# Kernel optimization log

Measured on AMD Instinct MI355X. Metric: run time of the kernel, lower is better.

Reference implementation:

```python
import jax, jax.numpy as jnp
import numpy as np
from jax import lax

EPS = 1e-10
DELU_P = 10.0

def delu(x):
    # delu_feature_map: param*relu(x) + (exp(param*min(x,0)) - 1) + 1
    x1 = jax.nn.relu(x)
    x2 = jnp.exp(DELU_P * (x - x1)) - 1.0
    return DELU_P * x1 + x2 + 1.0

def conv1x1(x, w, b):
    # x: (B,C,H,W), w: (O,C), b: (O,)
    return jnp.einsum('bchw,oc->bohw', x, w) + b[None, :, None, None]

def conv3x3(x, w, b):
    # w: (O,I,3,3), SAME padding, stride 1
    y = lax.conv_general_dilated(x, w, window_strides=(1, 1), padding='SAME',
                                 dimension_numbers=('NCHW', 'OIHW', 'NCHW'))
    return y + b[None, :, None, None]

def setup_inputs() -> dict:
    key = jax.random.key(0)
    ks = jax.random.split(key, 12)
    B, C, H, W = 4, 256, 128, 128
    s = 0.02
    return {
        'x':   jax.random.normal(ks[0], (B, C, H, W), dtype=jnp.float32),
        'wq':  jax.random.normal(ks[1], (C, C), dtype=jnp.float32) * s,
        'bq':  jax.random.normal(ks[2], (C,), dtype=jnp.float32) * s,
        'wk':  jax.random.normal(ks[3], (C, C), dtype=jnp.float32) * s,
        'bk':  jax.random.normal(ks[4], (C,), dtype=jnp.float32) * s,
        'wv':  jax.random.normal(ks[5], (C, C), dtype=jnp.float32) * s,
        'bv':  jax.random.normal(ks[6], (C,), dtype=jnp.float32) * s,
        'wd1': jax.random.normal(ks[7], (C, C), dtype=jnp.float32) * s,
        'bd1': jax.random.normal(ks[8], (C,), dtype=jnp.float32) * s,
        'wd3': jax.random.normal(ks[9], (C, C, 3, 3), dtype=jnp.float32) * s,
        'bd3': jax.random.normal(ks[10], (C,), dtype=jnp.float32) * s,
        'gamma': jax.random.normal(ks[11], (1,), dtype=jnp.float32) * 0.1,
    }

def reference(x, wq, bq, wk, bk, wv, bv, wd1, bd1, wd3, bd3, gamma):
    B, C, H, W = x.shape
    N = H * W
    # q/k/v projections flattened to (B, C, N)
    q = conv1x1(x, wq, bq).reshape(B, C, N)
    k = conv1x1(x, wk, bk).reshape(B, C, N)
    v = conv1x1(x, wv, bv).reshape(B, C, N)
    # feature maps (torch permutes q to (B,N,C), applies map, permutes back -> elementwise, no-op layout)
    q = delu(q)
    k = delu(k)
    # energy: (B, C, C), contracting over spatial N (q indexed 'bmn')
    energy = jnp.einsum('bmn,bcn->bmc', q, k)
    KV = k * v  # (B, C, N) elementwise
    norm = 1.0 / (jnp.einsum('bmc,bcn->bn', energy, k) + EPS)  # (B, N)
    # attention: sum over m of energy, times KV, times norm -> (B, C, N)
    attention = jnp.einsum('bmc,bcn,bn->bcn', energy, KV, norm)
    out = attention.reshape(B, C, H, W)
    out = out + conv1x1(x, wd1, bd1) + conv3x3(x, wd3, bd3)
    return x + gamma[0] * out
```

## Files before the change

### kernel.cpp

```cpp
#include <hip/hip_runtime.h>

#define BB 4
#define CC 256
#define HH 128
#define WW 128
#define NN (HH*WW)
#define EPSF 1e-10f

#define XR 130
#define XPB ((size_t)XR*XR*CC)

typedef __bf16 bf16x8 __attribute__((ext_vector_type(8)));
typedef float  f32x4  __attribute__((ext_vector_type(4)));
typedef float  f32x16 __attribute__((ext_vector_type(16)));

__device__ __forceinline__ float delu_f(float v) {
    return v > 0.0f ? fmaf(10.0f, v, 1.0f) : __expf(10.0f * v);
}

__device__ __forceinline__ void gl_lds16(const __bf16* g, __bf16* l) {
    __builtin_amdgcn_global_load_lds(
        (const __attribute__((address_space(1))) void*)g,
        (__attribute__((address_space(3))) void*)l, 16, 0, 0);
}

__global__ __launch_bounds__(256) void k_prep(const float* __restrict__ wq,
    const float* __restrict__ wk, const float* __restrict__ wv,
    const float* __restrict__ wd1, const float* __restrict__ wd3,
    __bf16* __restrict__ wqb, __bf16* __restrict__ wkb, __bf16* __restrict__ wvb,
    __bf16* __restrict__ wcv32)
{
    int idx = blockIdx.x * 256 + threadIdx.x;
    if (idx >= CC*CC) return;
    const int oc = idx >> 8, ic = idx & 255;
    const int ocf32 = oc >> 5;
    const int gks = ic >> 4, khi = (ic >> 3) & 1;
    const int lane32 = khi*32 + (oc & 31);
    const int e = ic & 7;
    const size_t off32 = ((size_t)(gks*8 + ocf32)*64 + lane32)*8 + e;
    wqb[off32] = (__bf16)wq[idx];
    wkb[off32] = (__bf16)wk[idx];
    wvb[off32] = (__bf16)wv[idx];
    float w9[9];
    #pragma unroll
    for (int k=0;k<9;k++) w9[k] = wd3[(size_t)idx*9 + k];
    w9[4] += wd1[idx];
    #pragma unroll
    for (int t=0;t<9;t++) wcv32[(size_t)t*CC*CC + off32] = (__bf16)w9[t];
}

__global__ __launch_bounds__(256) void k_xpad(const float* __restrict__ x,
                                              __bf16* __restrict__ xpad)
{
    const int xrow = blockIdx.x;
    const int b    = blockIdx.y;
    const int tid  = threadIdx.x;
    const int hr   = xrow - 1;
    const float* xb = x + (size_t)b*CC*NN;
    __bf16* xpb = xpad + (size_t)b*XPB + (size_t)xrow*XR*CC;
    const bool rowok = (hr >= 0 && hr < HH);
    for (int t = tid; t < XR*32; t += 256) {
        int xcol = t % XR, icg = t / XR;
        int wc = xcol - 1;
        bf16x8 v8 = {};
        if (rowok && wc >= 0 && wc < WW) {
            const float* p = xb + (size_t)(icg*8)*NN + hr*WW + wc;
            #pragma unroll
            for (int j=0;j<8;j++) v8[j] = (__bf16)p[(size_t)j*NN];
        }
        *(bf16x8*)&xpb[(size_t)xcol*CC + icg*8] = v8;
    }
}

__device__ __forceinline__ void stage_row128(const __bf16* __restrict__ xrb,
                                             __bf16* __restrict__ xs,
                                             int wid, int lane)
{
    #pragma unroll
    for (int j = 0; j < 16; ++j) {
        const int it = wid + 4*j;
        const int kq = it >> 1, ch = it & 1;
        gl_lds16(xrb + (size_t)(ch*64 + lane)*CC + kq*8, &xs[(size_t)(kq*132 + ch*64)*8]);
    }
}

__device__ __forceinline__ void mfma_gemm32(const __bf16* __restrict__ wb,
                                            const __bf16* __restrict__ xs,
                                            int wid, int lane, int l31, int lhi,
                                            f32x16 acc[2][4])
{
    #pragma unroll
    for (int kb=0; kb<8; kb++) {
        bf16x8 af[4];
        #pragma unroll
        for (int f=0; f<2; f++)
            #pragma unroll
            for (int kk=0; kk<2; kk++)
                af[f*2+kk] = *(const bf16x8*)&wb[((size_t)((kb*2+kk)*8 + wid*2 + f)*64 + lane)*8];
        #pragma unroll
        for (int kk=0; kk<2; kk++)
            #pragma unroll
            for (int nf=0; nf<4; nf++) {
                bf16x8 br = *(const bf16x8*)&xs[(size_t)((kb*4 + kk*2 + lhi)*132 + nf*32 + l31)*8];
                #pragma unroll
                for (int f=0; f<2; f++)
                    acc[f][nf] = __builtin_amdgcn_mfma_f32_32x32x16_bf16(af[f*2+kk], br, acc[f][nf], 0, 0, 0);
            }
    }
}

__global__ __launch_bounds__(256) void k_qk_mfma(const __bf16* __restrict__ xpad,
    const __bf16* __restrict__ wqb, const float* __restrict__ bq,
    const __bf16* __restrict__ wkb, const float* __restrict__ bk,
    __bf16* __restrict__ kp, float* __restrict__ Qs)
{
    __shared__ __bf16 xs[32*132*8];
    __shared__ float Qpart[4][128];
    const int h  = blockIdx.x;
    const int n0 = h * 128;
    const int b  = blockIdx.y;
    const int tid = threadIdx.x;
    const int wid = tid >> 6, lane = tid & 63;
    const int l31 = lane & 31, lhi = lane >> 5;
    const int oc_base = wid*64;
    const __bf16* xrb = xpad + (size_t)b*XPB + ((size_t)(h+1)*XR + 1)*CC;

    stage_row128(xrb, xs, wid, lane);
    __syncthreads();

    f32x16 acc[2][4] = {};
    mfma_gemm32(wqb, xs, wid, lane, l31, lhi, acc);
    #pragma unroll
    for (int nf=0; nf<4; nf++) {
        float s = 0.0f;
        #pragma unroll
        for (int f=0; f<2; f++)
            #pragma unroll
            for (int reg=0; reg<16; reg++) {
                const int oc = oc_base + f*32 + (reg&3) + 8*(reg>>2) + 4*lhi;
                s += delu_f(acc[f][nf][reg] + bq[oc]);
            }
        s += __shfl_xor(s, 32);
        if (lhi == 0) Qpart[wid][nf*32 + l31] = s;
    }
    __syncthreads();
    if (tid < 128)
        Qs[(size_t)b*NN + n0 + tid] = Qpart[0][tid] + Qpart[1][tid] + Qpart[2][tid] + Qpart[3][tid];

    #pragma unroll
    for (int f=0; f<2; f++)
        #pragma unroll
        for (int nf=0; nf<4; nf++)
            acc[f][nf] = (f32x16){};
    mfma_gemm32(wkb, xs, wid, lane, l31, lhi, acc);
    #pragma unroll
    for (int f=0; f<2; f++) {
        #pragma unroll
        for (int reg=0; reg<16; reg++) {
            const int oc = oc_base + f*32 + (reg&3) + 8*(reg>>2) + 4*lhi;
            const float bias = bk[oc];
            __bf16* kr = kp + ((size_t)b*CC + oc)*NN + n0;
            #pragma unroll
            for (int nf=0; nf<4; nf++)
                kr[nf*32 + l31] = (__bf16)delu_f(acc[f][nf][reg] + bias);
        }
    }
}

__global__ __launch_bounds__(256) void k_esum(const __bf16* __restrict__ kp,
    const float* __restrict__ Qs, float* __restrict__ Es)
{
    const int c = blockIdx.x & (CC-1), b = blockIdx.x >> 8;
    const int tid = threadIdx.x;
    const bf16x8* kr = (const bf16x8*)(kp + ((size_t)b*CC + c)*NN);
    const float4* qr = (const float4*)(Qs + (size_t)b*NN);
    float s = 0.0f;
    for (int i = tid; i < NN/8; i += 256) {
        bf16x8 kk = kr[i];
        float4 q0 = qr[2*i], q1 = qr[2*i+1];
        s += (float)kk[0]*q0.x + (float)kk[1]*q0.y + (float)kk[2]*q0.z + (float)kk[3]*q0.w
           + (float)kk[4]*q1.x + (float)kk[5]*q1.y + (float)kk[6]*q1.z + (float)kk[7]*q1.w;
    }
    #pragma unroll
    for (int m=1; m<64; m<<=1) s += __shfl_xor(s, m, 64);
    __shared__ float red[4];
    if ((tid & 63) == 0) red[tid >> 6] = s;
    __syncthreads();
    if (tid == 0) Es[b*CC + c] = red[0] + red[1] + red[2] + red[3];
}

__global__ __launch_bounds__(256,2) void k_conv_mfma(const __bf16* __restrict__ xpad,
    const __bf16* __restrict__ wcv32, const float* __restrict__ bd1,
    const float* __restrict__ bd3, __bf16* __restrict__ convout)
{
    __shared__ __bf16 xs[2][12*132*8];
    const int orig = blockIdx.x;
    const int wg   = (orig & 7)*64 + (orig >> 3);
    const int b    = wg >> 7;
    const int h    = wg & 127;
    const int tid = threadIdx.x;
    const int wid = tid >> 6, lane = tid & 63;
    const int l31 = lane & 31, lhi = lane >> 5;
    const int oc_base = wid*64;
    const __bf16* xpb = xpad + (size_t)b*XPB;

    f32x16 acc[2][4] = {};

    #define STAGE_CV(bufsel, icb) do {                                          \
        const int ic0_ = (icb)*32;                                              \
        _Pragma("unroll")                                                       \
        for (int j = 0; j < 9; ++j) {                                           \
            const int w_ = wid + 4*j;                                           \
            const int pair_ = w_ / 3, chunk_ = w_ % 3;                          \
            const int r_ = pair_ >> 2, icq_ = pair_ & 3;                        \
            const int col0_ = chunk_ * 64;                                      \
            if (col0_ + lane < XR)                                              \
                gl_lds16(xpb + ((size_t)(h + r_)*XR + col0_ + lane)*CC + ic0_ + icq_*8, \
                         &xs[bufsel][(size_t)(pair_*132 + col0_)*8]);           \
        }                                                                       \
    } while (0)

    #define AF_LOAD(dst, t, icb)                                                \
        _Pragma("unroll")                                                       \
        for (int f=0; f<2; f++)                                                 \
            _Pragma("unroll")                                                   \
            for (int kk=0; kk<2; kk++)                                          \
                dst[f*2+kk] = *(const bf16x8*)&wcv32[((size_t)(t)*CC*CC) +      \
                    ((size_t)((((icb)*2 + kk)*8 + wid*2 + f))*64 + lane)*8];

    STAGE_CV(0, 0);
    __syncthreads();

    #pragma unroll 1
    for (int icb = 0; icb < 8; ++icb) {
        bf16x8 af2[2][4];
        AF_LOAD(af2[0], 0, icb);
        if (icb < 7) STAGE_CV((icb+1)&1, icb+1);
        #pragma unroll
        for (int t=0; t<9; ++t) {
            const int cur = t & 1, nxt = cur ^ 1;
            const int ky = t/3, kx = t%3;
            if (t < 8) { AF_LOAD(af2[nxt], t+1, icb); }
            __builtin_amdgcn_s_setprio(1);
            #pragma unroll
            for (int kk=0; kk<2; kk++) {
                #pragma unroll
                for (int nf=0; nf<4; nf++) {
                    bf16x8 br = *(const bf16x8*)&xs[icb & 1][
                        (size_t)((ky*4 + kk*2 + lhi)*132 + nf*32 + l31 + kx)*8];
                    #pragma unroll
                    for (int f=0; f<2; f++)
                        acc[f][nf] = __builtin_amdgcn_mfma_f32_32x32x16_bf16(
                            af2[cur][f*2+kk], br, acc[f][nf], 0, 0, 0);
                }
            }
            __builtin_amdgcn_s_setprio(0);
        }
        __syncthreads();
    }
    #undef STAGE_CV
    #undef AF_LOAD

    #pragma unroll
    for (int f=0; f<2; f++) {
        #pragma unroll
        for (int reg=0; reg<16; reg++) {
            const int row = (reg & 3) + 8*(reg >> 2) + 4*lhi;
            const int oc = oc_base + f*32 + row;
            const float bias = bd1[oc] + bd3[oc];
            __bf16* orow = convout + ((size_t)b*CC + oc)*NN + (size_t)h*WW;
            #pragma unroll
            for (int nf=0; nf<4; nf++) {
                const int w = nf*32 + l31;
                orow[w] = (__bf16)(acc[f][nf][reg] + bias);
            }
        }
    }
}

__global__ __launch_bounds__(256) void k_vattn_mfma(
    const __bf16* __restrict__ xpad,
    const __bf16* __restrict__ wvb, const float* __restrict__ bv,
    const __bf16* __restrict__ kp, const float* __restrict__ Es,
    const __bf16* __restrict__ convout,
    const float* __restrict__ gamma, float* __restrict__ out)
{
    __shared__ __bf16 xs[32*132*8];
    __shared__ float Dpart[4][128];
    __shared__ float rn_sh[128];
    const int h  = blockIdx.x;
    const int n0 = h * 128;
    const int b  = blockIdx.y;
    const int tid = threadIdx.x;
    const int wid = tid >> 6, lane = tid & 63;
    const int l31 = lane & 31, lhi = lane >> 5;
    const int oc_base = wid*64;
    const __bf16* xrb = xpad + (size_t)b*XPB + ((size_t)(h+1)*XR + 1)*CC;

    stage_row128(xrb, xs, wid, lane);
    __syncthreads();

    f32x16 acc[2][4] = {};
    mfma_gemm32(wvb, xs, wid, lane, l31, lhi, acc);

    float dpart[4] = {0.f,0.f,0.f,0.f};
    #pragma unroll
    for (int f=0; f<2; f++) {
        #pragma unroll
        for (int reg=0; reg<16; reg++) {
            const int oc = oc_base + f*32 + (reg&3) + 8*(reg>>2) + 4*lhi;
            const float e = Es[b*CC + oc];
            const __bf16* kr = kp + ((size_t)b*CC + oc)*NN + n0;
            #pragma unroll
            for (int nf=0; nf<4; nf++)
                dpart[nf] = fmaf(e, (float)kr[nf*32 + l31], dpart[nf]);
        }
    }
    #pragma unroll
    for (int nf=0; nf<4; nf++) {
        dpart[nf] += __shfl_xor(dpart[nf], 32);
        if (lhi == 0) Dpart[wid][nf*32 + l31] = dpart[nf];
    }
    __syncthreads();
    if (tid < 128)
        rn_sh[tid] = 1.0f / (Dpart[0][tid] + Dpart[1][tid] + Dpart[2][tid] + Dpart[3][tid] + EPSF);
    __syncthreads();

    const float g = gamma[0];
    #pragma unroll
    for (int f=0; f<2; f++) {
        #pragma unroll
        for (int reg=0; reg<16; reg++) {
            const int oc = oc_base + f*32 + (reg&3) + 8*(reg>>2) + 4*lhi;
            const float eg = Es[b*CC + oc] * g;
            const float bias = bv[oc];
            const __bf16* kr = kp + ((size_t)b*CC + oc)*NN + n0;
            const __bf16* cr = convout + ((size_t)b*CC + oc)*NN + n0;
            const __bf16* xr = &xs[(size_t)((oc >> 3)*132)*8 + (oc & 7)];
            float* orow = out + ((size_t)b*CC + oc)*NN + n0;
            #pragma unroll
            for (int nf=0; nf<4; nf++) {
                const int w = nf*32 + l31;
                const float attn = eg*(float)kr[w]*rn_sh[w]*(acc[f][nf][reg] + bias);
                const float xv = (float)xr[(size_t)w*8];
                orow[w] = xv + attn + g*(float)cr[w];
            }
        }
    }
}

extern "C" void kernel_launch(void* const* d_in, const int* in_sizes, int n_in,
                              void* d_out, int out_size, void* d_ws, size_t ws_size,
                              hipStream_t stream)
{
    const float* x     = (const float*)d_in[0];
    const float* wq    = (const float*)d_in[1];
    const float* bq    = (const float*)d_in[2];
    const float* wk    = (const float*)d_in[3];
    const float* bk    = (const float*)d_in[4];
    const float* wv    = (const float*)d_in[5];
    const float* bv    = (const float*)d_in[6];
    const float* wd1   = (const float*)d_in[7];
    const float* bd1   = (const float*)d_in[8];
    const float* wd3   = (const float*)d_in[9];
    const float* bd3   = (const float*)d_in[10];
    const float* gamma = (const float*)d_in[11];
    float* out = (float*)d_out;

    __bf16* kp    = (__bf16*)d_ws;
    __bf16* cvout = kp + (size_t)BB*CC*NN;
    float*  Qs    = (float*)(cvout + (size_t)BB*CC*NN);
    float*  Es    = Qs + (size_t)BB*NN;
    __bf16* wcv32 = (__bf16*)(Es + (size_t)BB*CC);
    __bf16* wqb   = wcv32 + (size_t)9*CC*CC;
    __bf16* wkb   = wqb + (size_t)CC*CC;
    __bf16* wvb   = wkb + (size_t)CC*CC;
    __bf16* xpad  = wvb + (size_t)CC*CC;

    k_prep      <<<dim3(CC*CC/256), 256, 0, stream>>>(wq, wk, wv, wd1, wd3, wqb, wkb, wvb, wcv32);
    k_xpad      <<<dim3(XR, BB), 256, 0, stream>>>(x, xpad);
    k_qk_mfma   <<<dim3(HH, BB), 256, 0, stream>>>(xpad, wqb, bq, wkb, bk, kp, Qs);
    k_esum      <<<dim3(BB*CC), 256, 0, stream>>>(kp, Qs, Es);
    k_conv_mfma <<<dim3(HH*BB), 256, 0, stream>>>(xpad, wcv32, bd1, bd3, cvout);
    k_vattn_mfma<<<dim3(HH, BB), 256, 0, stream>>>(xpad, wvb, bv, kp, Es, cvout, gamma, out);
}
```

Before: 190.8 us.

## Run 3x3 conv in FP8 MFMA and store K feature map as FP8

Converts the fused 3x3+1x1 conv weights (scaled by 16) and the padded input to FP8 e4m3, and switches the conv GEMM to the 32x32x16 fp8 MFMA with half-size LDS staging. The delu'd K tensor is also stored as FP8 instead of bf16, which halves its write and read traffic in the qk, esum and vattn kernels. The aim is to cut conv compute and memory traffic. In exchange, k_xpad now writes an extra FP8 copy of the input, and the lower precision adds accuracy risk.

```diff
diff --git a/kernel.cpp b/kernel.cpp
--- a/kernel.cpp
+++ b/kernel.cpp
@@ -1,4 +1,5 @@
 #include <hip/hip_runtime.h>
+#include <hip/hip_fp8.h>
 
 #define BB 4
 #define CC 256
@@ -13,12 +14,16 @@
 typedef __bf16 bf16x8 __attribute__((ext_vector_type(8)));
 typedef float  f32x4  __attribute__((ext_vector_type(4)));
 typedef float  f32x16 __attribute__((ext_vector_type(16)));
+typedef unsigned char uchar;
 
 __device__ __forceinline__ float delu_f(float v) {
     return v > 0.0f ? fmaf(10.0f, v, 1.0f) : __expf(10.0f * v);
 }
 
-__device__ __forceinline__ void gl_lds16(const __bf16* g, __bf16* l) {
+__device__ __forceinline__ uchar fp8b(float f) { return __hip_fp8_e4m3(f).__x; }
+__device__ __forceinline__ float fp8f(uchar v) { __hip_fp8_e4m3 t; t.__x = v; return (float)t; }
+
+__device__ __forceinline__ void gl_lds16(const void* g, void* l) {
     __builtin_amdgcn_global_load_lds(
         (const __attribute__((address_space(1))) void*)g,
         (__attribute__((address_space(3))) void*)l, 16, 0, 0);
@@ -28,7 +33,7 @@
     const float* __restrict__ wk, const float* __restrict__ wv,
     const float* __restrict__ wd1, const float* __restrict__ wd3,
     __bf16* __restrict__ wqb, __bf16* __restrict__ wkb, __bf16* __restrict__ wvb,
-    __bf16* __restrict__ wcv32)
+    uchar* __restrict__ wcv8)
 {
     int idx = blockIdx.x * 256 + threadIdx.x;
     if (idx >= CC*CC) return;
@@ -46,29 +51,36 @@
     for (int k=0;k<9;k++) w9[k] = wd3[(size_t)idx*9 + k];
     w9[4] += wd1[idx];
     #pragma unroll
-    for (int t=0;t<9;t++) wcv32[(size_t)t*CC*CC + off32] = (__bf16)w9[t];
+    for (int t=0;t<9;t++) wcv8[(size_t)t*CC*CC + off32] = fp8b(w9[t] * 16.0f);
 }
 
 __global__ __launch_bounds__(256) void k_xpad(const float* __restrict__ x,
-                                              __bf16* __restrict__ xpad)
+                                              __bf16* __restrict__ xpad,
+                                              uchar* __restrict__ xpad8)
 {
     const int xrow = blockIdx.x;
     const int b    = blockIdx.y;
     const int tid  = threadIdx.x;
     const int hr   = xrow - 1;
     const float* xb = x + (size_t)b*CC*NN;
-    __bf16* xpb = xpad + (size_t)b*XPB + (size_t)xrow*XR*CC;
+    __bf16* xpb  = xpad  + (size_t)b*XPB + (size_t)xrow*XR*CC;
+    uchar*  xpb8 = xpad8 + (size_t)b*XPB + (size_t)xrow*XR*CC;
     const bool rowok = (hr >= 0 && hr < HH);
     for (int t = tid; t < XR*32; t += 256) {
         int xcol = t % XR, icg = t / XR;
         int wc = xcol - 1;
         bf16x8 v8 = {};
+        uchar u8[8] = {};
         if (rowok && wc >= 0 && wc < WW) {
             const float* p = xb + (size_t)(icg*8)*NN + hr*WW + wc;
             #pragma unroll
-            for (int j=0;j<8;j++) v8[j] = (__bf16)p[(size_t)j*NN];
+            for (int j=0;j<8;j++) { float f = p[(size_t)j*NN]; v8[j] = (__bf16)f; u8[j] = fp8b(f); }
         }
         *(bf16x8*)&xpb[(size_t)xcol*CC + icg*8] = v8;
+        unsigned long long pk = 0;
+        #pragma unroll
+        for (int j=0;j<8;j++) pk |= ((unsigned long long)u8[j]) << (8*j);
+        *(unsigned long long*)&xpb8[(size_t)xcol*CC + icg*8] = pk;
     }
 }
 
@@ -112,7 +124,7 @@
 __global__ __launch_bounds__(256) void k_qk_mfma(const __bf16* __restrict__ xpad,
     const __bf16* __restrict__ wqb, const float* __restrict__ bq,
     const __bf16* __restrict__ wkb, const float* __restrict__ bk,
-    __bf16* __restrict__ kp, float* __restrict__ Qs)
+    uchar* __restrict__ kp8, float* __restrict__ Qs)
 {
     __shared__ __bf16 xs[32*132*8];
     __shared__ float Qpart[4][128];
@@ -159,27 +171,29 @@
         for (int reg=0; reg<16; reg++) {
             const int oc = oc_base + f*32 + (reg&3) + 8*(reg>>2) + 4*lhi;
             const float bias = bk[oc];
-            __bf16* kr = kp + ((size_t)b*CC + oc)*NN + n0;
+            uchar* kr = kp8 + ((size_t)b*CC + oc)*NN + n0;
             #pragma unroll
             for (int nf=0; nf<4; nf++)
-                kr[nf*32 + l31] = (__bf16)delu_f(acc[f][nf][reg] + bias);
-        }
-    }
-}
-
-__global__ __launch_bounds__(256) void k_esum(const __bf16* __restrict__ kp,
+                kr[nf*32 + l31] = fp8b(delu_f(acc[f][nf][reg] + bias));
+        }
+    }
+}
+
+__global__ __launch_bounds__(256) void k_esum(const uchar* __restrict__ kp8,
     const float* __restrict__ Qs, float* __restrict__ Es)
 {
     const int c = blockIdx.x & (CC-1), b = blockIdx.x >> 8;
     const int tid = threadIdx.x;
-    const bf16x8* kr = (const bf16x8*)(kp + ((size_t)b*CC + c)*NN);
+    const uchar* kr = kp8 + ((size_t)b*CC + c)*NN;
     const float4* qr = (const float4*)(Qs + (size_t)b*NN);
     float s = 0.0f;
     for (int i = tid; i < NN/8; i += 256) {
-        bf16x8 kk = kr[i];
+        unsigned long long kkb = *(const unsigned long long*)&kr[(size_t)i*8];
         float4 q0 = qr[2*i], q1 = qr[2*i+1];
-        s += (float)kk[0]*q0.x + (float)kk[1]*q0.y + (float)kk[2]*q0.z + (float)kk[3]*q0.w
-           + (float)kk[4]*q1.x + (float)kk[5]*q1.y + (float)kk[6]*q1.z + (float)kk[7]*q1.w;
+        const float qv[8] = {q0.x,q0.y,q0.z,q0.w,q1.x,q1.y,q1.z,q1.w};
+        #pragma unroll
+        for (int j=0;j<8;j++)
+            s = fmaf(fp8f((uchar)(kkb >> (8*j))), qv[j], s);
     }
     #pragma unroll
     for (int m=1; m<64; m<<=1) s += __shfl_xor(s, m, 64);
@@ -189,11 +203,11 @@
     if (tid == 0) Es[b*CC + c] = red[0] + red[1] + red[2] + red[3];
 }
 
-__global__ __launch_bounds__(256,2) void k_conv_mfma(const __bf16* __restrict__ xpad,
-    const __bf16* __restrict__ wcv32, const float* __restrict__ bd1,
+__global__ __launch_bounds__(256,2) void k_conv_mfma(const uchar* __restrict__ xpad8,
+    const uchar* __restrict__ wcv8, const float* __restrict__ bd1,
     const float* __restrict__ bd3, __bf16* __restrict__ convout)
 {
-    __shared__ __bf16 xs[2][12*132*8];
+    __shared__ uchar xs8[2][6*132*16];
     const int orig = blockIdx.x;
     const int wg   = (orig & 7)*64 + (orig >> 3);
     const int b    = wg >> 7;
@@ -202,64 +216,66 @@
     const int wid = tid >> 6, lane = tid & 63;
     const int l31 = lane & 31, lhi = lane >> 5;
     const int oc_base = wid*64;
-    const __bf16* xpb = xpad + (size_t)b*XPB;
+    const uchar* xpb8 = xpad8 + (size_t)b*XPB;
 
     f32x16 acc[2][4] = {};
 
-    #define STAGE_CV(bufsel, icb) do {                                          \
+    #define STAGE_CV8(bufsel, icb) do {                                         \
         const int ic0_ = (icb)*32;                                              \
         _Pragma("unroll")                                                       \
-        for (int j = 0; j < 9; ++j) {                                           \
+        for (int j = 0; j < 5; ++j) {                                           \
             const int w_ = wid + 4*j;                                           \
-            const int pair_ = w_ / 3, chunk_ = w_ % 3;                          \
-            const int r_ = pair_ >> 2, icq_ = pair_ & 3;                        \
-            const int col0_ = chunk_ * 64;                                      \
-            if (col0_ + lane < XR)                                              \
-                gl_lds16(xpb + ((size_t)(h + r_)*XR + col0_ + lane)*CC + ic0_ + icq_*8, \
-                         &xs[bufsel][(size_t)(pair_*132 + col0_)*8]);           \
+            if (w_ < 18) {                                                      \
+                const int pair_ = w_ / 3, chunk_ = w_ % 3;                      \
+                const int r_ = pair_ >> 1, g16_ = pair_ & 1;                    \
+                const int col0_ = chunk_ * 64;                                  \
+                if (col0_ + lane < XR)                                          \
+                    gl_lds16(xpb8 + ((size_t)(h + r_)*XR + col0_ + lane)*CC + ic0_ + g16_*16, \
+                             &xs8[bufsel][(size_t)(pair_*132 + col0_)*16]);     \
+            }                                                                   \
         }                                                                       \
     } while (0)
 
-    #define AF_LOAD(dst, t, icb)                                                \
+    #define AF8_LOAD(dst, t, icb)                                               \
         _Pragma("unroll")                                                       \
         for (int f=0; f<2; f++)                                                 \
             _Pragma("unroll")                                                   \
             for (int kk=0; kk<2; kk++)                                          \
-                dst[f*2+kk] = *(const bf16x8*)&wcv32[((size_t)(t)*CC*CC) +      \
+                dst[f*2+kk] = *(const long*)&wcv8[(size_t)(t)*CC*CC +           \
                     ((size_t)((((icb)*2 + kk)*8 + wid*2 + f))*64 + lane)*8];
 
-    STAGE_CV(0, 0);
+    STAGE_CV8(0, 0);
     __syncthreads();
 
     #pragma unroll 1
     for (int icb = 0; icb < 8; ++icb) {
-        bf16x8 af2[2][4];
-        AF_LOAD(af2[0], 0, icb);
-        if (icb < 7) STAGE_CV((icb+1)&1, icb+1);
+        long af8[2][4];
+        AF8_LOAD(af8[0], 0, icb);
+        if (icb < 7) STAGE_CV8((icb+1)&1, icb+1);
         #pragma unroll
         for (int t=0; t<9; ++t) {
             const int cur = t & 1, nxt = cur ^ 1;
             const int ky = t/3, kx = t%3;
-            if (t < 8) { AF_LOAD(af2[nxt], t+1, icb); }
+            if (t < 8) { AF8_LOAD(af8[nxt], t+1, icb); }
             __builtin_amdgcn_s_setprio(1);
             #pragma unroll
             for (int kk=0; kk<2; kk++) {
                 #pragma unroll
                 for (int nf=0; nf<4; nf++) {
-                    bf16x8 br = *(const bf16x8*)&xs[icb & 1][
-                        (size_t)((ky*4 + kk*2 + lhi)*132 + nf*32 + l31 + kx)*8];
+                    long br = *(const long*)&xs8[icb & 1][
+                        (size_t)((ky*2 + kk)*132 + nf*32 + l31 + kx)*16 + lhi*8];
                     #pragma unroll
                     for (int f=0; f<2; f++)
-                        acc[f][nf] = __builtin_amdgcn_mfma_f32_32x32x16_bf16(
-                            af2[cur][f*2+kk], br, acc[f][nf], 0, 0, 0);
+                        acc[f][nf] = __builtin_amdgcn_mfma_f32_32x32x16_fp8_fp8(
+                            af8[cur][f*2+kk], br, acc[f][nf], 0, 0, 0);
                 }
             }
             __builtin_amdgcn_s_setprio(0);
         }
         __syncthreads();
     }
-    #undef STAGE_CV
-    #undef AF_LOAD
+    #undef STAGE_CV8
+    #undef AF8_LOAD
 
     #pragma unroll
     for (int f=0; f<2; f++) {
@@ -272,7 +288,7 @@
             #pragma unroll
             for (int nf=0; nf<4; nf++) {
                 const int w = nf*32 + l31;
-                orow[w] = (__bf16)(acc[f][nf][reg] + bias);
+                orow[w] = (__bf16)(acc[f][nf][reg]*0.0625f + bias);
             }
         }
     }
@@ -281,7 +297,7 @@
 __global__ __launch_bounds__(256) void k_vattn_mfma(
     const __bf16* __restrict__ xpad,
     const __bf16* __restrict__ wvb, const float* __restrict__ bv,
-    const __bf16* __restrict__ kp, const float* __restrict__ Es,
+    const uchar* __restrict__ kp8, const float* __restrict__ Es,
     const __bf16* __restrict__ convout,
     const float* __restrict__ gamma, float* __restrict__ out)
 {
@@ -310,10 +326,10 @@
         for (int reg=0; reg<16; reg++) {
             const int oc = oc_base + f*32 + (reg&3) + 8*(reg>>2) + 4*lhi;
             const float e = Es[b*CC + oc];
-            const __bf16* kr = kp + ((size_t)b*CC + oc)*NN + n0;
+            const uchar* kr = kp8 + ((size_t)b*CC + oc)*NN + n0;
             #pragma unroll
             for (int nf=0; nf<4; nf++)
-                dpart[nf] = fmaf(e, (float)kr[nf*32 + l31], dpart[nf]);
+                dpart[nf] = fmaf(e, fp8f(kr[nf*32 + l31]), dpart[nf]);
         }
     }
     #pragma unroll
@@ -334,14 +350,14 @@
             const int oc = oc_base + f*32 + (reg&3) + 8*(reg>>2) + 4*lhi;
             const float eg = Es[b*CC + oc] * g;
             const float bias = bv[oc];
-            const __bf16* kr = kp + ((size_t)b*CC + oc)*NN + n0;
+            const uchar*  kr = kp8 + ((size_t)b*CC + oc)*NN + n0;
             const __bf16* cr = convout + ((size_t)b*CC + oc)*NN + n0;
             const __bf16* xr = &xs[(size_t)((oc >> 3)*132)*8 + (oc & 7)];
             float* orow = out + ((size_t)b*CC + oc)*NN + n0;
             #pragma unroll
             for (int nf=0; nf<4; nf++) {
                 const int w = nf*32 + l31;
-                const float attn = eg*(float)kr[w]*rn_sh[w]*(acc[f][nf][reg] + bias);
+                const float attn = eg*fp8f(kr[w])*rn_sh[w]*(acc[f][nf][reg] + bias);
                 const float xv = (float)xr[(size_t)w*8];
                 orow[w] = xv + attn + g*(float)cr[w];
             }
@@ -367,20 +383,21 @@
     const float* gamma = (const float*)d_in[11];
     float* out = (float*)d_out;
 
-    __bf16* kp    = (__bf16*)d_ws;
-    __bf16* cvout = kp + (size_t)BB*CC*NN;
+    uchar*  kp8   = (uchar*)d_ws;
+    __bf16* cvout = (__bf16*)(kp8 + (size_t)BB*CC*NN);
     float*  Qs    = (float*)(cvout + (size_t)BB*CC*NN);
     float*  Es    = Qs + (size_t)BB*NN;
-    __bf16* wcv32 = (__bf16*)(Es + (size_t)BB*CC);
-    __bf16* wqb   = wcv32 + (size_t)9*CC*CC;
+    uchar*  wcv8  = (uchar*)(Es + (size_t)BB*CC);
+    __bf16* wqb   = (__bf16*)(wcv8 + (size_t)9*CC*CC);
     __bf16* wkb   = wqb + (size_t)CC*CC;
     __bf16* wvb   = wkb + (size_t)CC*CC;
     __bf16* xpad  = wvb + (size_t)CC*CC;
-
-    k_prep      <<<dim3(CC*CC/256), 256, 0, stream>>>(wq, wk, wv, wd1, wd3, wqb, wkb, wvb, wcv32);
-    k_xpad      <<<dim3(XR, BB), 256, 0, stream>>>(x, xpad);
-    k_qk_mfma   <<<dim3(HH, BB), 256, 0, stream>>>(xpad, wqb, bq, wkb, bk, kp, Qs);
-    k_esum      <<<dim3(BB*CC), 256, 0, stream>>>(kp, Qs, Es);
-    k_conv_mfma <<<dim3(HH*BB), 256, 0, stream>>>(xpad, wcv32, bd1, bd3, cvout);
-    k_vattn_mfma<<<dim3(HH, BB), 256, 0, stream>>>(xpad, wvb, bv, kp, Es, cvout, gamma, out);
-}
+    uchar*  xpad8 = (uchar*)(xpad + (size_t)BB*XPB);
+
+    k_prep      <<<dim3(CC*CC/256), 256, 0, stream>>>(wq, wk, wv, wd1, wd3, wqb, wkb, wvb, wcv8);
+    k_xpad      <<<dim3(XR, BB), 256, 0, stream>>>(x, xpad, xpad8);
+    k_qk_mfma   <<<dim3(HH, BB), 256, 0, stream>>>(xpad, wqb, bq, wkb, bk, kp8, Qs);
+    k_esum      <<<dim3(BB*CC), 256, 0, stream>>>(kp8, Qs, Es);
+    k_conv_mfma <<<dim3(HH*BB), 256, 0, stream>>>(xpad8, wcv8, bd1, bd3, cvout);
+    k_vattn_mfma<<<dim3(HH, BB), 256, 0, stream>>>(xpad, wvb, bv, kp8, Es, cvout, gamma, out);
+}
```

Measured after the change: 197.2 us. 3.4% more time.
